# Kernel tuning notes

Hardware: AMD Instinct MI355X
Metric: run time of the kernel (lower is better)

The kernel has to match this reference:

```python
import jax, jax.numpy as jnp
import numpy as np

K = 3          # pooling factor (init k)
H_OUT = 8      # number of bilinear heads
H_DIM = 512    # hidden dim after pooling
BN_EPS = 1e-5
NEG_INF = -jnp.inf


def setup_inputs() -> dict:
    key = jax.random.key(0)
    ks = jax.random.split(key, 8)
    b, vn, qn, vd, qd = 16, 256, 256, 512, 768
    hk = H_DIM * K
    return {
        "v": jax.random.normal(ks[0], (b, vn, vd), jnp.float32),
        "q": jax.random.normal(ks[1], (b, qn, qd), jnp.float32),
        "Wv": jax.random.normal(ks[2], (hk, vd), jnp.float32) * 0.05,
        "bv": jax.random.normal(ks[3], (hk,), jnp.float32) * 0.05,
        "Wq": jax.random.normal(ks[4], (hk, qd), jnp.float32) * 0.05,
        "bq": jax.random.normal(ks[5], (hk,), jnp.float32) * 0.05,
        "h_mat": jax.random.normal(ks[6], (1, H_OUT, 1, hk), jnp.float32),
        "h_bias": jax.random.normal(ks[7], (1, H_OUT, 1, 1), jnp.float32),
        "bn_gamma": jnp.ones((H_DIM,), jnp.float32),
        "bn_beta": jnp.zeros((H_DIM,), jnp.float32),
    }


def _forward(v, q, Wv, bv, Wq, bq, h_mat, h_bias, bn_gamma, bn_beta):
    # FCNet (eval mode: dropout is identity; weight_norm folded into W)
    v_ = jax.nn.relu(jnp.einsum("bvd,kd->bvk", v, Wv) + bv)   # [b, vn, h_dim*k]
    q_ = jax.nn.relu(jnp.einsum("bqd,kd->bqk", q, Wq) + bq)   # [b, qn, h_dim*k]

    # Bilinear attention maps: [b, h_out, vn, qn]
    att = jnp.einsum("xhyk,bvk,bqk->bhvq", h_mat, v_, q_) + h_bias

    # v_mask / q_mask (all-zero token rows masked to -inf)
    v_zero = jnp.sum(jnp.abs(v), axis=2) == 0                  # [b, vn]
    q_zero = jnp.sum(jnp.abs(q), axis=2) == 0                  # [b, qn]
    att = jnp.where(v_zero[:, None, :, None], NEG_INF, att)
    att = jnp.where(q_zero[:, None, None, :], NEG_INF, att)

    # Fused per-head attention pooling, summed over heads (original Python loop)
    fused = jnp.einsum("bhvq,bqk->bhvk", att, q_)
    logits_k = jnp.einsum("bvk,bhvk->bk", v_, fused)           # [b, h_dim*k]

    # AvgPool1d(k, stride=k) * k  == sum over groups of k
    b = logits_k.shape[0]
    logits = logits_k.reshape(b, H_DIM, K).sum(axis=2)         # [b, h_dim]

    # BatchNorm1d (training-mode batch statistics, biased variance)
    mu = logits.mean(axis=0)
    var = logits.var(axis=0)
    logits = (logits - mu) * jax.lax.rsqrt(var + BN_EPS) * bn_gamma + bn_beta
    return logits, att


def reference(v, q, Wv, bv, Wq, bq, h_mat, h_bias, bn_gamma, bn_beta):
    return _forward(v, q, Wv, bv, Wq, bq, h_mat, h_bias, bn_gamma, bn_beta)
```

## Files before the change

kernel.cpp:

```cpp
#include <hip/hip_runtime.h>
#include <math.h>

#define BB    16
#define VN    256
#define QN    256
#define VD    512
#define QD    768
#define HK    1536
#define HDIM  512

typedef _Float16 half8 __attribute__((ext_vector_type(8)));
typedef _Float16 half4 __attribute__((ext_vector_type(4)));
typedef float f32x4 __attribute__((ext_vector_type(4)));

__global__ __launch_bounds__(256) void conv_mask2(
    const float* __restrict__ v, const float* __restrict__ q,
    _Float16* __restrict__ v16, _Float16* __restrict__ q16,
    float* __restrict__ vz, float* __restrict__ qz) {
    int which = blockIdx.y;
    const float* src = which ? q : v;
    _Float16* dst = which ? q16 : v16;
    float* outz = which ? qz : vz;
    int D = which ? QD : VD;
    int w = threadIdx.x >> 6, ln = threadIdx.x & 63;
    int row = blockIdx.x * 4 + w;
    const float* p = src + (size_t)row * D;
    _Float16* d = dst + (size_t)row * D;
    float s = 0.f;
    for (int c = ln * 4; c < D; c += 256) {
        float4 x = *(const float4*)(p + c);
        s += fabsf(x.x) + fabsf(x.y) + fabsf(x.z) + fabsf(x.w);
        half4 hh = {(_Float16)x.x, (_Float16)x.y, (_Float16)x.z, (_Float16)x.w};
        *(half4*)(d + c) = hh;
    }
    for (int off = 32; off > 0; off >>= 1) s += __shfl_down(s, off);
    if (ln == 0) outz[row] = (s == 0.f) ? 1.f : 0.f;
}

__global__ __launch_bounds__(256) void conv_w3(
    const float* __restrict__ Wv, _Float16* __restrict__ Wv16, int n4v,
    const float* __restrict__ Wq, _Float16* __restrict__ Wq16, int n4q,
    const float* __restrict__ hm, _Float16* __restrict__ hs16) {
    if (blockIdx.y == 2) {
        int k = blockIdx.x * 256 + threadIdx.x;
        if (k >= HK) return;
        float s = 0.f;
#pragma unroll
        for (int h = 0; h < 8; ++h) {
            float x = hm[h * HK + k];
            s += x;
            hs16[h * HK + k] = (_Float16)x;
        }
        hs16[8 * HK + k] = (_Float16)s;
        return;
    }
    const float* src = blockIdx.y ? Wq : Wv;
    _Float16* dst = blockIdx.y ? Wq16 : Wv16;
    int n4 = blockIdx.y ? n4q : n4v;
    int i = blockIdx.x * 256 + threadIdx.x;
    if (i < n4) {
        float4 x = ((const float4*)src)[i];
        half4 h = {(_Float16)x.x, (_Float16)x.y, (_Float16)x.z, (_Float16)x.w};
        ((half4*)dst)[i] = h;
    }
}

__global__ __launch_bounds__(128) void proj_lds(
    const _Float16* __restrict__ Ain, const _Float16* __restrict__ W16,
    const float* __restrict__ bias, _Float16* __restrict__ C16, int K) {
    __shared__ _Float16 As[64 * 64];
    __shared__ _Float16 Bs[64 * 64];
    int m0 = blockIdx.y * 64, n0 = blockIdx.x * 64;
    int t = threadIdx.x;
    int w = t >> 6, ln = t & 63, quad = ln >> 4, r16 = ln & 15;
    int arow = t >> 3, aseg = t & 7;
    int sg = aseg ^ (arow & 7);
    const _Float16* ApG = Ain + (size_t)(m0 + arow) * K + aseg * 8;
    const _Float16* BpG = W16 + (size_t)(n0 + arow) * K + aseg * 8;
    half8 ra[4], rb[4];
#pragma unroll
    for (int c = 0; c < 4; ++c) {
        ra[c] = *(const half8*)(ApG + (size_t)c * 16 * K);
        rb[c] = *(const half8*)(BpG + (size_t)c * 16 * K);
    }
    f32x4 acc[2][4] = {};
    for (int k0 = 0; k0 < K; k0 += 64) {
        __syncthreads();
#pragma unroll
        for (int c = 0; c < 4; ++c) {
            *(half8*)&As[(c * 16 + arow) * 64 + sg * 8] = ra[c];
            *(half8*)&Bs[(c * 16 + arow) * 64 + sg * 8] = rb[c];
        }
        __syncthreads();
        if (k0 + 64 < K) {
#pragma unroll
            for (int c = 0; c < 4; ++c) {
                ra[c] = *(const half8*)(ApG + (size_t)c * 16 * K + k0 + 64);
                rb[c] = *(const half8*)(BpG + (size_t)c * 16 * K + k0 + 64);
            }
        }
#pragma unroll
        for (int kc = 0; kc < 2; ++kc) {
            half8 af[2], bf[4];
#pragma unroll
            for (int fi = 0; fi < 2; ++fi) {
                int rl = w * 32 + fi * 16 + r16;
                af[fi] = *(const half8*)&As[rl * 64 + ((kc * 4 + quad) ^ (rl & 7)) * 8];
            }
#pragma unroll
            for (int fj = 0; fj < 4; ++fj) {
                int rl = fj * 16 + r16;
                bf[fj] = *(const half8*)&Bs[rl * 64 + ((kc * 4 + quad) ^ (rl & 7)) * 8];
            }
#pragma unroll
            for (int fi = 0; fi < 2; ++fi)
#pragma unroll
                for (int fj = 0; fj < 4; ++fj)
                    acc[fi][fj] = __builtin_amdgcn_mfma_f32_16x16x32_f16(
                        af[fi], bf[fj], acc[fi][fj], 0, 0, 0);
        }
    }
#pragma unroll
    for (int fi = 0; fi < 2; ++fi) {
#pragma unroll
        for (int r = 0; r < 4; ++r) {
            int m = m0 + w * 32 + fi * 16 + quad * 4 + r;
#pragma unroll
            for (int fj = 0; fj < 4; ++fj) {
                int n = n0 + fj * 16 + r16;
                float x = acc[fi][fj][r] + bias[n];
                C16[(size_t)m * HK + n] = (_Float16)fmaxf(x, 0.f);
            }
        }
    }
}

__global__ __launch_bounds__(256) void att4(
    const _Float16* __restrict__ v16, const _Float16* __restrict__ q16,
    const _Float16* __restrict__ hs16, const float* __restrict__ hb,
    const float* __restrict__ vz, const float* __restrict__ qz,
    float* __restrict__ att_out, _Float16* __restrict__ A16) {
    __shared__ _Float16 As[64 * 64];
    __shared__ _Float16 Bs[64 * 64];
    __shared__ _Float16 Hl[3 * HK];
    int z = blockIdx.z;
    int b = z / 3, hg = z - b * 3;
    int h0 = hg * 3;
    int i0 = blockIdx.y * 64, j0 = blockIdx.x * 64;
    int t = threadIdx.x;
    int w = t >> 6, ln = t & 63, quad = ln >> 4, r16 = ln & 15;
    int wi = w & 1, wj = w >> 1;
    int arow = t >> 3, aseg = t & 7;
    int sg = aseg ^ (arow & 7);
    for (int u = t * 8; u < 3 * HK; u += 256 * 8)
        *(half8*)&Hl[u] = *(const half8*)(hs16 + (size_t)h0 * HK + u);
    const _Float16* ApG = v16 + (size_t)b * VN * HK + (size_t)(i0 + arow) * HK + aseg * 8;
    const _Float16* BpG = q16 + (size_t)b * QN * HK + (size_t)(j0 + arow) * HK + aseg * 8;
    half8 ra[2], rb[2];
#pragma unroll
    for (int c = 0; c < 2; ++c) {
        ra[c] = *(const half8*)(ApG + (size_t)c * 32 * HK);
        rb[c] = *(const half8*)(BpG + (size_t)c * 32 * HK);
    }
    f32x4 acc[3][2][2] = {};
    for (int it = 0; it < 24; ++it) {
        __syncthreads();
#pragma unroll
        for (int c = 0; c < 2; ++c) {
            *(half8*)&As[(c * 32 + arow) * 64 + sg * 8] = ra[c];
            *(half8*)&Bs[(c * 32 + arow) * 64 + sg * 8] = rb[c];
        }
        __syncthreads();
        if (it + 1 < 24) {
            int kn = (it + 1) * 64;
#pragma unroll
            for (int c = 0; c < 2; ++c) {
                ra[c] = *(const half8*)(ApG + (size_t)c * 32 * HK + kn);
                rb[c] = *(const half8*)(BpG + (size_t)c * 32 * HK + kn);
            }
        }
        int kb = it * 64;
#pragma unroll
        for (int kc = 0; kc < 2; ++kc) {
            half8 af[2], bf[2];
#pragma unroll
            for (int fi = 0; fi < 2; ++fi) {
                int rl = wi * 32 + fi * 16 + r16;
                af[fi] = *(const half8*)&As[rl * 64 + ((kc * 4 + quad) ^ (rl & 7)) * 8];
            }
#pragma unroll
            for (int fj = 0; fj < 2; ++fj) {
                int rl = wj * 32 + fj * 16 + r16;
                bf[fj] = *(const half8*)&Bs[rl * 64 + ((kc * 4 + quad) ^ (rl & 7)) * 8];
            }
#pragma unroll
            for (int hh = 0; hh < 3; ++hh) {
                half8 hmv = *(const half8*)&Hl[hh * HK + kb + (kc * 4 + quad) * 8];
#pragma unroll
                for (int fi = 0; fi < 2; ++fi) {
                    half8 am = af[fi] * hmv;
#pragma unroll
                    for (int fj = 0; fj < 2; ++fj)
                        acc[hh][fi][fj] = __builtin_amdgcn_mfma_f32_16x16x32_f16(
                            am, bf[fj], acc[hh][fi][fj], 0, 0, 0);
                }
            }
        }
    }
#pragma unroll
    for (int hh = 0; hh < 3; ++hh) {
        int h = h0 + hh;
        float hbv;
        if (h < 8) {
            hbv = hb[h];
        } else {
            hbv = 0.f;
#pragma unroll
            for (int x = 0; x < 8; ++x) hbv += hb[x];
        }
        if (h < 8) {
            float* outb = att_out + ((size_t)(b * 8 + h)) * VN * QN;
#pragma unroll
            for (int fi = 0; fi < 2; ++fi) {
#pragma unroll
                for (int r = 0; r < 4; ++r) {
                    int i = i0 + wi * 32 + fi * 16 + quad * 4 + r;
                    float vm = vz[b * VN + i];
#pragma unroll
                    for (int fj = 0; fj < 2; ++fj) {
                        int j = j0 + wj * 32 + fj * 16 + r16;
                        float x = acc[hh][fi][fj][r] + hbv;
                        if (vm != 0.f || qz[b * QN + j] != 0.f) x = -INFINITY;
                        outb[(size_t)i * QN + j] = x;
                    }
                }
            }
        } else {
            _Float16* Ab = A16 + (size_t)b * VN * QN;
#pragma unroll
            for (int fi = 0; fi < 2; ++fi) {
#pragma unroll
                for (int r = 0; r < 4; ++r) {
                    int i = i0 + wi * 32 + fi * 16 + quad * 4 + r;
                    float vm = vz[b * VN + i];
#pragma unroll
                    for (int fj = 0; fj < 2; ++fj) {
                        int j = j0 + wj * 32 + fj * 16 + r16;
                        float x = acc[hh][fi][fj][r] + hbv;
                        if (vm != 0.f || qz[b * QN + j] != 0.f) x = -INFINITY;
                        Ab[(size_t)i * QN + j] = (_Float16)x;
                    }
                }
            }
        }
    }
}

__global__ __launch_bounds__(256) void transpose_q16(const _Float16* __restrict__ q16,
                                                     _Float16* __restrict__ q16t) {
    __shared__ _Float16 Ls[32][72];
    int b = blockIdx.z;
    int k0 = blockIdx.x * 64, j0 = blockIdx.y * 32;
    int t = threadIdx.x;
    const _Float16* src = q16 + (size_t)b * QN * HK;
    int tj = t >> 3, tk = (t & 7) * 8;
    half8 vv = *(const half8*)(src + (size_t)(j0 + tj) * HK + k0 + tk);
#pragma unroll
    for (int e = 0; e < 8; ++e) Ls[tj][tk + e] = vv[e];
    __syncthreads();
    int ok = t >> 2, oj = (t & 3) * 8;
    half8 ov;
#pragma unroll
    for (int e = 0; e < 8; ++e) ov[e] = Ls[oj + e][ok];
    *(half8*)(q16t + (size_t)b * HK * QN + (size_t)(k0 + ok) * QN + j0 + oj) = ov;
}

__global__ __launch_bounds__(256) void t_lk_mfma(
    const _Float16* __restrict__ A16, const _Float16* __restrict__ q16t,
    const _Float16* __restrict__ v16, float* __restrict__ lk) {
    __shared__ _Float16 As[256 * 32];
    __shared__ _Float16 Bs[64 * 32];
    __shared__ float red[16][64];
    int b = blockIdx.y;
    int k0 = blockIdx.x * 64;
    int t = threadIdx.x;
    int w = t >> 6, ln = t & 63, quad = ln >> 4, r16 = ln & 15;
    const _Float16* Ab = A16 + (size_t)b * VN * QN;
    const _Float16* Qt = q16t + (size_t)b * HK * QN + (size_t)k0 * QN;
    int ar = t >> 2, aseg = t & 3;
    f32x4 acc[4][4] = {};
    for (int j0 = 0; j0 < QN; j0 += 32) {
        half8 a0 = *(const half8*)(Ab + (size_t)(ar +   0) * QN + j0 + aseg * 8);
        half8 a1 = *(const half8*)(Ab + (size_t)(ar +  64) * QN + j0 + aseg * 8);
        half8 a2 = *(const half8*)(Ab + (size_t)(ar + 128) * QN + j0 + aseg * 8);
        half8 a3 = *(const half8*)(Ab + (size_t)(ar + 192) * QN + j0 + aseg * 8);
        half8 bv = *(const half8*)(Qt + (size_t)ar * QN + j0 + aseg * 8);
        __syncthreads();
        *(half8*)&As[(ar +   0) * 32 + aseg * 8] = a0;
        *(half8*)&As[(ar +  64) * 32 + aseg * 8] = a1;
        *(half8*)&As[(ar + 128) * 32 + aseg * 8] = a2;
        *(half8*)&As[(ar + 192) * 32 + aseg * 8] = a3;
        *(half8*)&Bs[ar * 32 + aseg * 8] = bv;
        __syncthreads();
        half8 af[4], bf[4];
#pragma unroll
        for (int fi = 0; fi < 4; ++fi)
            af[fi] = *(const half8*)&As[(w * 64 + fi * 16 + r16) * 32 + quad * 8];
#pragma unroll
        for (int fj = 0; fj < 4; ++fj)
            bf[fj] = *(const half8*)&Bs[(fj * 16 + r16) * 32 + quad * 8];
#pragma unroll
        for (int fi = 0; fi < 4; ++fi)
#pragma unroll
            for (int fj = 0; fj < 4; ++fj)
                acc[fi][fj] = __builtin_amdgcn_mfma_f32_16x16x32_f16(
                    af[fi], bf[fj], acc[fi][fj], 0, 0, 0);
    }
    const _Float16* Vb = v16 + (size_t)b * VN * HK;
    float part[4] = {0.f, 0.f, 0.f, 0.f};
#pragma unroll
    for (int fi = 0; fi < 4; ++fi) {
#pragma unroll
        for (int r = 0; r < 4; ++r) {
            int i = w * 64 + fi * 16 + quad * 4 + r;
#pragma unroll
            for (int fj = 0; fj < 4; ++fj) {
                float vv = (float)Vb[(size_t)i * HK + k0 + fj * 16 + r16];
                part[fj] += acc[fi][fj][r] * vv;
            }
        }
    }
#pragma unroll
    for (int fj = 0; fj < 4; ++fj)
        red[w * 4 + quad][fj * 16 + r16] = part[fj];
    __syncthreads();
    if (t < 64) {
        float s = 0.f;
#pragma unroll
        for (int g = 0; g < 16; ++g) s += red[g][t];
        lk[b * HK + k0 + t] = s;
    }
}

__global__ __launch_bounds__(256) void bn_kernel(
    const float* __restrict__ lk, const float* __restrict__ gamma,
    const float* __restrict__ beta, float* __restrict__ out) {
    int d = blockIdx.x * blockDim.x + threadIdx.x;
    if (d >= HDIM) return;
    float l[BB];
    float mu = 0.f;
#pragma unroll
    for (int b = 0; b < BB; ++b) {
        const float* p = lk + b * HK + 3 * d;
        float s = p[0] + p[1] + p[2];
        l[b] = s;
        mu += s;
    }
    mu *= (1.f / BB);
    float var = 0.f;
#pragma unroll
    for (int b = 0; b < BB; ++b) {
        float dd = l[b] - mu;
        var += dd * dd;
    }
    var *= (1.f / BB);
    float inv = rsqrtf(var + 1e-5f);
    float g = gamma[d], be = beta[d];
#pragma unroll
    for (int b = 0; b < BB; ++b)
        out[b * HDIM + d] = (l[b] - mu) * inv * g + be;
}

extern "C" void kernel_launch(void* const* d_in, const int* in_sizes, int n_in,
                              void* d_out, int out_size, void* d_ws, size_t ws_size,
                              hipStream_t stream) {
    const float* v  = (const float*)d_in[0];
    const float* q  = (const float*)d_in[1];
    const float* Wv = (const float*)d_in[2];
    const float* bv = (const float*)d_in[3];
    const float* Wq = (const float*)d_in[4];
    const float* bq = (const float*)d_in[5];
    const float* hm = (const float*)d_in[6];
    const float* hb = (const float*)d_in[7];
    const float* gamma = (const float*)d_in[8];
    const float* beta  = (const float*)d_in[9];

    float* out_logits = (float*)d_out;
    float* out_att    = out_logits + BB * HDIM;

    _Float16* h = (_Float16*)d_ws;
    _Float16* v16   = h;
    _Float16* q16   = v16 + (size_t)BB * VN * HK;
    _Float16* q16t  = q16 + (size_t)BB * QN * HK;
    _Float16* A16   = q16t + (size_t)BB * HK * QN;
    _Float16* v16in = A16 + (size_t)BB * VN * QN;
    _Float16* q16in = v16in + (size_t)BB * VN * VD;
    _Float16* Wv16  = q16in + (size_t)BB * QN * QD;
    _Float16* Wq16  = Wv16 + (size_t)HK * VD;
    _Float16* hs16  = Wq16 + (size_t)HK * QD;
    float* lk = (float*)(hs16 + 9 * HK + 8);
    float* vz = lk + BB * HK;
    float* qz = vz + BB * VN;

    conv_mask2<<<dim3(BB * VN / 4, 2), 256, 0, stream>>>(v, q, v16in, q16in, vz, qz);
    conv_w3<<<dim3((HK * QD / 4 + 255) / 256, 3), 256, 0, stream>>>(
        Wv, Wv16, HK * VD / 4, Wq, Wq16, HK * QD / 4, hm, hs16);

    proj_lds<<<dim3(HK / 64, BB * VN / 64), 128, 0, stream>>>(v16in, Wv16, bv, v16, VD);
    proj_lds<<<dim3(HK / 64, BB * QN / 64), 128, 0, stream>>>(q16in, Wq16, bq, q16, QD);

    att4<<<dim3(QN / 64, VN / 64, BB * 3), 256, 0, stream>>>(
        v16, q16, hs16, hb, vz, qz, out_att, A16);

    transpose_q16<<<dim3(HK / 64, QN / 32, BB), 256, 0, stream>>>(q16, q16t);

    t_lk_mfma<<<dim3(HK / 64, BB), 256, 0, stream>>>(A16, q16t, v16, lk);

    bn_kernel<<<dim3((HDIM + 255) / 256), 256, 0, stream>>>(lk, gamma, beta, out_logits);
}
```

Measured before the change: 202.2 us.

## Compute all eight heads per block and derive summed head from accumulators

The attention kernel now computes all eight heads in one block over a 64x32 tile with 128 threads, replacing the three-head-group split that spent a ninth 'summed head' on extra MFMA work. The summed attention map used for pooling is now obtained by adding the eight head accumulators in the epilogue, which removes one head's worth of matrix work and the repeated loads of v/q tiles across head groups. In exchange each thread holds 8x2x2 accumulators, which raises register pressure, and the LDS for the head weights grows to 8*HK halves. The grid also shrinks in its head dimension.

```diff
diff --git a/kernel.cpp b/kernel.cpp
--- a/kernel.cpp
+++ b/kernel.cpp
@@ -135,49 +135,49 @@
     }
 }
 
-__global__ __launch_bounds__(256) void att4(
+__global__ __launch_bounds__(128, 2) void att8(
     const _Float16* __restrict__ v16, const _Float16* __restrict__ q16,
     const _Float16* __restrict__ hs16, const float* __restrict__ hb,
     const float* __restrict__ vz, const float* __restrict__ qz,
     float* __restrict__ att_out, _Float16* __restrict__ A16) {
     __shared__ _Float16 As[64 * 64];
-    __shared__ _Float16 Bs[64 * 64];
-    __shared__ _Float16 Hl[3 * HK];
-    int z = blockIdx.z;
-    int b = z / 3, hg = z - b * 3;
-    int h0 = hg * 3;
-    int i0 = blockIdx.y * 64, j0 = blockIdx.x * 64;
+    __shared__ _Float16 Bs[32 * 64];
+    __shared__ _Float16 Hl[8 * HK];
+    int b = blockIdx.z;
+    int i0 = blockIdx.y * 64, j0 = blockIdx.x * 32;
     int t = threadIdx.x;
     int w = t >> 6, ln = t & 63, quad = ln >> 4, r16 = ln & 15;
-    int wi = w & 1, wj = w >> 1;
     int arow = t >> 3, aseg = t & 7;
     int sg = aseg ^ (arow & 7);
-    for (int u = t * 8; u < 3 * HK; u += 256 * 8)
-        *(half8*)&Hl[u] = *(const half8*)(hs16 + (size_t)h0 * HK + u);
+    for (int u = t * 8; u < 8 * HK; u += 128 * 8)
+        *(half8*)&Hl[u] = *(const half8*)(hs16 + u);
     const _Float16* ApG = v16 + (size_t)b * VN * HK + (size_t)(i0 + arow) * HK + aseg * 8;
     const _Float16* BpG = q16 + (size_t)b * QN * HK + (size_t)(j0 + arow) * HK + aseg * 8;
-    half8 ra[2], rb[2];
-#pragma unroll
-    for (int c = 0; c < 2; ++c) {
-        ra[c] = *(const half8*)(ApG + (size_t)c * 32 * HK);
-        rb[c] = *(const half8*)(BpG + (size_t)c * 32 * HK);
-    }
-    f32x4 acc[3][2][2] = {};
+    half8 ra[4], rb[2];
+#pragma unroll
+    for (int c = 0; c < 4; ++c)
+        ra[c] = *(const half8*)(ApG + (size_t)c * 16 * HK);
+#pragma unroll
+    for (int c = 0; c < 2; ++c)
+        rb[c] = *(const half8*)(BpG + (size_t)c * 16 * HK);
+    f32x4 acc[8][2][2] = {};
     for (int it = 0; it < 24; ++it) {
         __syncthreads();
 #pragma unroll
-        for (int c = 0; c < 2; ++c) {
-            *(half8*)&As[(c * 32 + arow) * 64 + sg * 8] = ra[c];
-            *(half8*)&Bs[(c * 32 + arow) * 64 + sg * 8] = rb[c];
-        }
+        for (int c = 0; c < 4; ++c)
+            *(half8*)&As[(c * 16 + arow) * 64 + sg * 8] = ra[c];
+#pragma unroll
+        for (int c = 0; c < 2; ++c)
+            *(half8*)&Bs[(c * 16 + arow) * 64 + sg * 8] = rb[c];
         __syncthreads();
         if (it + 1 < 24) {
             int kn = (it + 1) * 64;
 #pragma unroll
-            for (int c = 0; c < 2; ++c) {
-                ra[c] = *(const half8*)(ApG + (size_t)c * 32 * HK + kn);
-                rb[c] = *(const half8*)(BpG + (size_t)c * 32 * HK + kn);
-            }
+            for (int c = 0; c < 4; ++c)
+                ra[c] = *(const half8*)(ApG + (size_t)c * 16 * HK + kn);
+#pragma unroll
+            for (int c = 0; c < 2; ++c)
+                rb[c] = *(const half8*)(BpG + (size_t)c * 16 * HK + kn);
         }
         int kb = it * 64;
 #pragma unroll
@@ -185,16 +185,16 @@
             half8 af[2], bf[2];
 #pragma unroll
             for (int fi = 0; fi < 2; ++fi) {
-                int rl = wi * 32 + fi * 16 + r16;
+                int rl = w * 32 + fi * 16 + r16;
                 af[fi] = *(const half8*)&As[rl * 64 + ((kc * 4 + quad) ^ (rl & 7)) * 8];
             }
 #pragma unroll
             for (int fj = 0; fj < 2; ++fj) {
-                int rl = wj * 32 + fj * 16 + r16;
+                int rl = fj * 16 + r16;
                 bf[fj] = *(const half8*)&Bs[rl * 64 + ((kc * 4 + quad) ^ (rl & 7)) * 8];
             }
 #pragma unroll
-            for (int hh = 0; hh < 3; ++hh) {
+            for (int hh = 0; hh < 8; ++hh) {
                 half8 hmv = *(const half8*)&Hl[hh * HK + kb + (kc * 4 + quad) * 8];
 #pragma unroll
                 for (int fi = 0; fi < 2; ++fi) {
@@ -207,50 +207,39 @@
             }
         }
     }
-#pragma unroll
-    for (int hh = 0; hh < 3; ++hh) {
-        int h = h0 + hh;
-        float hbv;
-        if (h < 8) {
-            hbv = hb[h];
-        } else {
-            hbv = 0.f;
-#pragma unroll
-            for (int x = 0; x < 8; ++x) hbv += hb[x];
-        }
-        if (h < 8) {
-            float* outb = att_out + ((size_t)(b * 8 + h)) * VN * QN;
-#pragma unroll
-            for (int fi = 0; fi < 2; ++fi) {
-#pragma unroll
-                for (int r = 0; r < 4; ++r) {
-                    int i = i0 + wi * 32 + fi * 16 + quad * 4 + r;
-                    float vm = vz[b * VN + i];
-#pragma unroll
-                    for (int fj = 0; fj < 2; ++fj) {
-                        int j = j0 + wj * 32 + fj * 16 + r16;
-                        float x = acc[hh][fi][fj][r] + hbv;
-                        if (vm != 0.f || qz[b * QN + j] != 0.f) x = -INFINITY;
-                        outb[(size_t)i * QN + j] = x;
-                    }
+    float hbs[8];
+    float hbsum = 0.f;
+#pragma unroll
+    for (int h = 0; h < 8; ++h) {
+        hbs[h] = hb[h];
+        hbsum += hbs[h];
+    }
+    float qm[2];
+#pragma unroll
+    for (int fj = 0; fj < 2; ++fj)
+        qm[fj] = qz[b * QN + j0 + fj * 16 + r16];
+#pragma unroll
+    for (int fi = 0; fi < 2; ++fi) {
+#pragma unroll
+        for (int r = 0; r < 4; ++r) {
+            int i = i0 + w * 32 + fi * 16 + quad * 4 + r;
+            float vm = vz[b * VN + i];
+#pragma unroll
+            for (int fj = 0; fj < 2; ++fj) {
+                int j = j0 + fj * 16 + r16;
+                bool msk = (vm != 0.f) || (qm[fj] != 0.f);
+                float s = 0.f;
+#pragma unroll
+                for (int h = 0; h < 8; ++h) {
+                    float a = acc[h][fi][fj][r];
+                    s += a;
+                    float x = a + hbs[h];
+                    if (msk) x = -INFINITY;
+                    att_out[((size_t)(b * 8 + h)) * VN * QN + (size_t)i * QN + j] = x;
                 }
-            }
-        } else {
-            _Float16* Ab = A16 + (size_t)b * VN * QN;
-#pragma unroll
-            for (int fi = 0; fi < 2; ++fi) {
-#pragma unroll
-                for (int r = 0; r < 4; ++r) {
-                    int i = i0 + wi * 32 + fi * 16 + quad * 4 + r;
-                    float vm = vz[b * VN + i];
-#pragma unroll
-                    for (int fj = 0; fj < 2; ++fj) {
-                        int j = j0 + wj * 32 + fj * 16 + r16;
-                        float x = acc[hh][fi][fj][r] + hbv;
-                        if (vm != 0.f || qz[b * QN + j] != 0.f) x = -INFINITY;
-                        Ab[(size_t)i * QN + j] = (_Float16)x;
-                    }
-                }
+                float xs = s + hbsum;
+                if (msk) xs = -INFINITY;
+                A16[(size_t)b * VN * QN + (size_t)i * QN + j] = (_Float16)xs;
             }
         }
     }
@@ -409,7 +398,7 @@
     proj_lds<<<dim3(HK / 64, BB * VN / 64), 128, 0, stream>>>(v16in, Wv16, bv, v16, VD);
     proj_lds<<<dim3(HK / 64, BB * QN / 64), 128, 0, stream>>>(q16in, Wq16, bq, q16, QD);
 
-    att4<<<dim3(QN / 64, VN / 64, BB * 3), 256, 0, stream>>>(
+    att8<<<dim3(QN / 32, VN / 64, BB), 128, 0, stream>>>(
         v16, q16, hs16, hb, vz, qz, out_att, A16);
 
     transpose_q16<<<dim3(HK / 64, QN / 32, BB), 256, 0, stream>>>(q16, q16t);
```

Result: no change. 198.8 us (-1.7%).
